# Optimization experiments

Hardware: AMD Instinct MI355X
Metric: run time of the kernel (lower is better)

The kernel has to match this reference:

```python
import jax, jax.numpy as jnp
import numpy as np

# Model constants (match init_kwargs + mamba_ssm defaults)
CIN, COUT, K, STRIDE = 64, 128, 4, 4
D = 128            # d_model = features_out
DI = 256           # d_inner = 2*D (expand=2)
NSTATE = 16        # d_state
DCONV = 4          # depthwise conv width
DT_RANK = 8        # ceil(D/16)
NB = 3             # blocks per direction
NTOT = 2 * NB      # forward + backward stacks


def setup_inputs() -> dict:
    key = jax.random.key(0)
    ks = jax.random.split(key, 10)
    s = 0.02
    x = jax.random.normal(ks[0], (2, CIN, 8192), jnp.float32)
    convd_w = jax.random.normal(ks[1], (COUT, CIN, K), jnp.float32) * s
    convd_b = jnp.zeros((COUT,), jnp.float32)
    ln_w = jnp.ones((NTOT, D), jnp.float32)
    ln_b = jnp.zeros((NTOT, D), jnp.float32)
    in_proj_w = jax.random.normal(ks[2], (NTOT, 2 * DI, D), jnp.float32) * s
    conv_w = jax.random.normal(ks[3], (NTOT, DI, DCONV), jnp.float32) * s
    conv_b = jnp.zeros((NTOT, DI), jnp.float32)
    xproj_w = jax.random.normal(ks[4], (NTOT, DT_RANK + 2 * NSTATE, DI), jnp.float32) * s
    dtproj_w = jax.random.normal(ks[5], (NTOT, DI, DT_RANK), jnp.float32) * s
    dtproj_b = jax.random.normal(ks[6], (NTOT, DI), jnp.float32) * s
    # S4D-real init: A = -[1..N]
    A_log = jnp.log(jnp.broadcast_to(jnp.arange(1, NSTATE + 1, dtype=jnp.float32), (NTOT, DI, NSTATE)))
    Dparam = jnp.ones((NTOT, DI), jnp.float32)
    outproj_w = jax.random.normal(ks[7], (NTOT, D, DI), jnp.float32) * s
    return dict(x=x, convd_w=convd_w, convd_b=convd_b, ln_w=ln_w, ln_b=ln_b,
                in_proj_w=in_proj_w, conv_w=conv_w, conv_b=conv_b, xproj_w=xproj_w,
                dtproj_w=dtproj_w, dtproj_b=dtproj_b, A_log=A_log, Dparam=Dparam,
                outproj_w=outproj_w)


def _silu(x):
    return x * jax.nn.sigmoid(x)


def _layernorm(x, w, b, eps=1e-5):
    m = x.mean(-1, keepdims=True)
    xc = x - m
    v = (xc * xc).mean(-1, keepdims=True)
    return xc * jax.lax.rsqrt(v + eps) * w + b


def _mamba_mixer(x, in_proj_w, conv_w, conv_b, xproj_w, dtproj_w, dtproj_b, A_log, Dp, outproj_w):
    # x: (B, L, D)
    B, L, _ = x.shape
    xz = jnp.einsum('bld,ed->ble', x, in_proj_w)          # (B, L, 2*DI)
    xm, z = jnp.split(xz, 2, axis=-1)
    # causal depthwise conv (pad left DCONV-1, truncate to L)
    xp = jnp.pad(xm, ((0, 0), (DCONV - 1, 0), (0, 0)))
    xc = conv_b
    acc = jnp.zeros_like(xm)
    for k in range(DCONV):
        acc = acc + xp[:, k:k + L, :] * conv_w[:, k]
    xc = _silu(acc + conv_b)                               # (B, L, DI)
    dbc = jnp.einsum('ble,ne->bln', xc, xproj_w)           # (B, L, DT_RANK + 2N)
    dt, Bc, Cc = jnp.split(dbc, [DT_RANK, DT_RANK + NSTATE], axis=-1)
    dt = jax.nn.softplus(jnp.einsum('blr,dr->bld', dt, dtproj_w) + dtproj_b)  # (B, L, DI)
    A = -jnp.exp(A_log)                                    # (DI, N)
    dA = jnp.exp(dt[..., None] * A)                        # (B, L, DI, N)
    dBx = dt[..., None] * Bc[:, :, None, :] * xc[..., None]

    def step(h, inp):
        dA_t, dBx_t, C_t = inp
        h = dA_t * h + dBx_t                               # (B, DI, N)
        y = jnp.einsum('bdn,bn->bd', h, C_t)
        return h, y

    h0 = jnp.zeros((B, DI, NSTATE), x.dtype)
    _, ys = jax.lax.scan(step, h0, (jnp.swapaxes(dA, 0, 1), jnp.swapaxes(dBx, 0, 1), jnp.swapaxes(Cc, 0, 1)))
    y = jnp.swapaxes(ys, 0, 1)                             # (B, L, DI)
    y = (y + Dp * xc) * _silu(z)
    return jnp.einsum('ble,de->bld', y, outproj_w)         # (B, L, D)


def _mamba_stack(x, off, ln_w, ln_b, in_proj_w, conv_w, conv_b, xproj_w, dtproj_w, dtproj_b, A_log, Dparam, outproj_w):
    # mamba_ssm Block semantics: residual = x (+ prev residual); x = mixer(norm(residual))
    res = None
    cur = x
    for i in range(NB):
        j = off + i
        res = cur if res is None else cur + res
        hn = _layernorm(res, ln_w[j], ln_b[j])
        cur = _mamba_mixer(hn, in_proj_w[j], conv_w[j], conv_b[j], xproj_w[j],
                           dtproj_w[j], dtproj_b[j], A_log[j], Dparam[j], outproj_w[j])
    return cur, res


def reference(x, convd_w, convd_b, ln_w, ln_b, in_proj_w, conv_w, conv_b, xproj_w,
              dtproj_w, dtproj_b, A_log, Dparam, outproj_w):
    # downsampling conv + SiLU
    y = jax.lax.conv_general_dilated(x, convd_w, (STRIDE,), 'VALID',
                                     dimension_numbers=('NCH', 'OIH', 'NCH'))
    y = _silu(y + convd_b[None, :, None])                  # (B, COUT, L')
    h = jnp.swapaxes(y, 1, 2)                              # (B, L', D)
    xf, rf = _mamba_stack(h, 0, ln_w, ln_b, in_proj_w, conv_w, conv_b, xproj_w,
                          dtproj_w, dtproj_b, A_log, Dparam, outproj_w)
    xb, rb = _mamba_stack(h[:, ::-1, :], NB, ln_w, ln_b, in_proj_w, conv_w, conv_b, xproj_w,
                          dtproj_w, dtproj_b, A_log, Dparam, outproj_w)
    out = (xf + rf) + (xb + rb)[:, ::-1, :]
    return jnp.swapaxes(out, 1, 2), rf, rb
```

## Files before the change

### kernel.cpp

```cpp
#include <hip/hip_runtime.h>
#include <hip/hip_bf16.h>
#include <math.h>

#define B    2
#define CIN  64
#define LIN  8192
#define L    2048
#define D    128
#define DI   256
#define NS   16
#define RK   8
#define NSTREAM 4
#define CH   32
#define NCH  (L/CH)
#define TOK  (NSTREAM*L)
#define SZ_D ((size_t)TOK*D)
#define SZ_DI ((size_t)TOK*DI)
#define SXM 280
#define SHN 152

typedef short  bfrag __attribute__((ext_vector_type(8)));
typedef float  facc  __attribute__((ext_vector_type(4)));
#define MFMA __builtin_amdgcn_mfma_f32_16x16x32_bf16

__device__ __forceinline__ float sigmoidf_(float x){ return 1.f/(1.f+__expf(-x)); }
__device__ __forceinline__ float siluf_(float x){ return x*sigmoidf_(x); }
__device__ __forceinline__ ushort f2bf(float f){
    unsigned u = __float_as_uint(f);
    u += 0x7fffu + ((u>>16)&1u);
    return (ushort)(u>>16);
}
__device__ __forceinline__ float bf2f(ushort u){ return __uint_as_float(((unsigned)u)<<16); }
__device__ __forceinline__ float softplusf_(float t){
    return (t > 20.f) ? t : __logf(1.f + __expf(t));
}

__global__ void k_cvtall(const float* __restrict__ cw, const float* __restrict__ ipw,
                         const float* __restrict__ opw, const float* __restrict__ xpw,
                         ushort* __restrict__ dst){
    int i = blockIdx.x*256 + threadIdx.x;
    ushort v;
    if (i < 32768)       v = f2bf(cw[i]);
    else if (i < 425984) v = f2bf(ipw[i-32768]);
    else if (i < 622592) v = f2bf(opw[i-425984]);
    else {
        int t = i - 622592;
        int k = t & 255, nr = (t>>8) & 63, j = t>>14;
        v = (nr < 40) ? f2bf(xpw[((size_t)j*40 + nr)*256 + k]) : (ushort)0;
    }
    dst[i] = v;
}

__global__ void k_down(const float* __restrict__ x, const ushort* __restrict__ wd,
                       const float* __restrict__ bias, float* __restrict__ h){
    __shared__ ushort sxd[64*SXM];
    int tid = threadIdx.x;
    int m0 = blockIdx.x*64;
    int b = m0 >> 11;
    int l0 = m0 & 2047;
    for (int idx = tid; idx < 64*64; idx += 256){
        int t = idx & 63, cc = idx >> 6;
        float4 v = *(const float4*)(x + ((size_t)(b*CIN + cc))*LIN + 4*(l0+t));
        ushort4 o; o.x=f2bf(v.x); o.y=f2bf(v.y); o.z=f2bf(v.z); o.w=f2bf(v.w);
        *(ushort4*)&sxd[t*SXM + cc*4] = o;
    }
    __syncthreads();
    int w = tid>>6, lane = tid&63, rw = w>>1, cw = w&1;
    int q = lane>>4, r = lane&15;
    int n0 = blockIdx.y*64 + cw*32;
    const ushort* b0p = wd + (size_t)(n0 + r)*256 + q*8;
    const ushort* b1p = b0p + (size_t)16*256;
    facc acc[2][2] = {};
    #pragma unroll
    for (int kb=0; kb<8; ++kb){
        bfrag a0 = *(bfrag*)&sxd[(rw*32 + r)*SXM + kb*32 + q*8];
        bfrag a1 = *(bfrag*)&sxd[(rw*32 + 16 + r)*SXM + kb*32 + q*8];
        bfrag b0 = *(const bfrag*)(b0p + kb*32);
        bfrag b1 = *(const bfrag*)(b1p + kb*32);
        acc[0][0] = MFMA(a0,b0,acc[0][0],0,0,0);
        acc[0][1] = MFMA(a0,b1,acc[0][1],0,0,0);
        acc[1][0] = MFMA(a1,b0,acc[1][0],0,0,0);
        acc[1][1] = MFMA(a1,b1,acc[1][1],0,0,0);
    }
    #pragma unroll
    for (int im=0; im<2; ++im)
    #pragma unroll
    for (int in=0; in<2; ++in){
        int col = n0 + in*16 + r;
        float bv = bias[col];
        #pragma unroll
        for (int r2=0; r2<4; ++r2){
            int row = m0 + rw*32 + im*16 + q*4 + r2;
            int bb = row >> 11, l = row & 2047;
            float v = siluf_(acc[im][in][r2] + bv);
            h[((size_t)(bb*L + l))*D + col] = v;
            h[((size_t)((2+bb)*L + (L-1-l)))*D + col] = v;
        }
    }
}

__global__ void __launch_bounds__(256,1)
k_head(const float* __restrict__ curIn, const float* __restrict__ resIn,
       float* __restrict__ resOut,
       const float* __restrict__ lnw, const float* __restrict__ lnb,
       const ushort* __restrict__ wbi, const ushort* __restrict__ wbx,
       const float* __restrict__ cw, const float* __restrict__ cb,
       const float* __restrict__ Wdt, const float* __restrict__ bdt,
       const float* __restrict__ A_log,
       float* __restrict__ z, float* __restrict__ xc,
       float* __restrict__ dtr, float* __restrict__ Bc, float* __restrict__ Cc,
       float* __restrict__ Aprod, float* __restrict__ Bend, int blk, int first){
    __shared__ ushort smHn[35*SHN];
    __shared__ ushort smXm[35*SXM];
    __shared__ ushort smXc[32*SXM];
    __shared__ float  smDbc[32*68];
    const int tid = threadIdx.x;
    const int bi = blockIdx.x;
    const int s = bi >> 6, c = bi & 63;
    const int j = (s>>1)*3 + blk;
    const int base_tok = s*L + c*CH;

    {
        int t = tid >> 3, g8 = tid & 7;
        size_t off = (size_t)(base_tok + t)*D + g8*16;
        float4 v[4];
        const float4* cp = (const float4*)(curIn + off);
        #pragma unroll
        for (int i=0;i<4;++i) v[i] = cp[i];
        if (!first){
            const float4* rp = (const float4*)(resIn + off);
            #pragma unroll
            for (int i=0;i<4;++i){ float4 rv=rp[i]; v[i].x+=rv.x; v[i].y+=rv.y; v[i].z+=rv.z; v[i].w+=rv.w; }
        }
        {
            float4* ro = (float4*)(resOut + off);
            #pragma unroll
            for (int i=0;i<4;++i) ro[i] = v[i];
        }
        float s1=0.f, s2=0.f;
        #pragma unroll
        for (int i=0;i<4;++i){
            s1 += v[i].x+v[i].y+v[i].z+v[i].w;
            s2 += v[i].x*v[i].x+v[i].y*v[i].y+v[i].z*v[i].z+v[i].w*v[i].w;
        }
        s1 += __shfl_xor(s1,1); s2 += __shfl_xor(s2,1);
        s1 += __shfl_xor(s1,2); s2 += __shfl_xor(s2,2);
        s1 += __shfl_xor(s1,4); s2 += __shfl_xor(s2,4);
        float mean = s1*(1.f/128.f);
        float var  = s2*(1.f/128.f) - mean*mean;
        float rstd = rsqrtf(var + 1e-5f);
        const float4* lwp = (const float4*)(lnw + j*D + g8*16);
        const float4* lbp = (const float4*)(lnb + j*D + g8*16);
        #pragma unroll
        for (int i=0;i<4;++i){
            float4 lw = lwp[i], lb = lbp[i];
            ushort4 o;
            o.x = f2bf((v[i].x-mean)*rstd*lw.x + lb.x);
            o.y = f2bf((v[i].y-mean)*rstd*lw.y + lb.y);
            o.z = f2bf((v[i].z-mean)*rstd*lw.z + lb.z);
            o.w = f2bf((v[i].w-mean)*rstd*lw.w + lb.w);
            *(ushort4*)&smHn[t*SHN + g8*16 + i*4] = o;
        }
    }
    if (c > 0 && tid < 24){
        int t = tid >> 3, g8 = tid & 7;
        size_t off = (size_t)(base_tok - 3 + t)*D + g8*16;
        float4 v[4];
        const float4* cp = (const float4*)(curIn + off);
        #pragma unroll
        for (int i=0;i<4;++i) v[i] = cp[i];
        if (!first){
            const float4* rp = (const float4*)(resIn + off);
            #pragma unroll
            for (int i=0;i<4;++i){ float4 rv=rp[i]; v[i].x+=rv.x; v[i].y+=rv.y; v[i].z+=rv.z; v[i].w+=rv.w; }
        }
        float s1=0.f, s2=0.f;
        #pragma unroll
        for (int i=0;i<4;++i){
            s1 += v[i].x+v[i].y+v[i].z+v[i].w;
            s2 += v[i].x*v[i].x+v[i].y*v[i].y+v[i].z*v[i].z+v[i].w*v[i].w;
        }
        s1 += __shfl_xor(s1,1); s2 += __shfl_xor(s2,1);
        s1 += __shfl_xor(s1,2); s2 += __shfl_xor(s2,2);
        s1 += __shfl_xor(s1,4); s2 += __shfl_xor(s2,4);
        float mean = s1*(1.f/128.f);
        float var  = s2*(1.f/128.f) - mean*mean;
        float rstd = rsqrtf(var + 1e-5f);
        const float4* lwp = (const float4*)(lnw + j*D + g8*16);
        const float4* lbp = (const float4*)(lnb + j*D + g8*16);
        #pragma unroll
        for (int i=0;i<4;++i){
            float4 lw = lwp[i], lb = lbp[i];
            ushort4 o;
            o.x = f2bf((v[i].x-mean)*rstd*lw.x + lb.x);
            o.y = f2bf((v[i].y-mean)*rstd*lw.y + lb.y);
            o.z = f2bf((v[i].z-mean)*rstd*lw.z + lb.z);
            o.w = f2bf((v[i].w-mean)*rstd*lw.w + lb.w);
            *(ushort4*)&smHn[(32+t)*SHN + g8*16 + i*4] = o;
        }
    }
    __syncthreads();

    {
        int w = tid>>6, lane = tid&63, q = lane>>4, r = lane&15;
        bfrag a[3][4];
        #pragma unroll
        for (int rt=0; rt<3; ++rt)
        #pragma unroll
        for (int kb=0; kb<4; ++kb)
            a[rt][kb] = *(bfrag*)&smHn[(rt*16 + r)*SHN + kb*32 + q*8];
        #pragma unroll
        for (int ct=0; ct<8; ++ct){
            int n0 = w*128 + ct*16;
            const ushort* bp = wbi + ((size_t)j*512 + n0 + r)*128 + q*8;
            facc a0 = {}, a1 = {}, a2 = {};
            #pragma unroll
            for (int kb=0; kb<4; ++kb){
                bfrag bv = *(const bfrag*)(bp + kb*32);
                a0 = MFMA(a[0][kb], bv, a0, 0,0,0);
                a1 = MFMA(a[1][kb], bv, a1, 0,0,0);
                a2 = MFMA(a[2][kb], bv, a2, 0,0,0);
            }
            int colL = n0 + r;
            if (colL < DI){
                #pragma unroll
                for (int r2=0;r2<4;++r2){
                    int rr = q*4 + r2;
                    smXm[rr*SXM + colL]      = f2bf(a0[r2]);
                    smXm[(16+rr)*SXM + colL] = f2bf(a1[r2]);
                    if (rr < 3) smXm[(32+rr)*SXM + colL] = f2bf(a2[r2]);
                }
            } else {
                int cz = colL - DI;
                #pragma unroll
                for (int r2=0;r2<4;++r2){
                    int rr = q*4 + r2;
                    z[(size_t)(base_tok + rr)*DI + cz]      = a0[r2];
                    z[(size_t)(base_tok + 16 + rr)*DI + cz] = a1[r2];
                }
            }
        }
    }
    __syncthreads();

    {
        const float* w4 = cw + ((size_t)j*DI + tid)*4;
        float cw0=w4[0], cw1=w4[1], cw2=w4[2], cw3=w4[3];
        float cbb = cb[j*DI + tid];
        float xm1=0.f, xm2=0.f, xm3=0.f;
        if (c > 0){
            xm3 = bf2f(smXm[32*SXM + tid]);
            xm2 = bf2f(smXm[33*SXM + tid]);
            xm1 = bf2f(smXm[34*SXM + tid]);
        }
        #pragma unroll 4
        for (int i=0;i<CH;++i){
            float x0 = bf2f(smXm[i*SXM + tid]);
            float v = siluf_(cbb + cw3*x0 + cw2*xm1 + cw1*xm2 + cw0*xm3);
            smXc[i*SXM + tid] = f2bf(v);
            xc[(size_t)(base_tok+i)*DI + tid] = v;
            xm3 = xm2; xm2 = xm1; xm1 = x0;
        }
    }
    __syncthreads();

    {
        int w = tid>>6, lane = tid&63, q = lane>>4, r = lane&15;
        facc a0 = {}, a1 = {};
        const ushort* bp = wbx + ((size_t)j*64 + w*16 + r)*256 + q*8;
        #pragma unroll
        for (int kb=0; kb<8; ++kb){
            bfrag av0 = *(bfrag*)&smXc[r*SXM + kb*32 + q*8];
            bfrag av1 = *(bfrag*)&smXc[(16+r)*SXM + kb*32 + q*8];
            bfrag bv  = *(const bfrag*)(bp + kb*32);
            a0 = MFMA(av0, bv, a0, 0,0,0);
            a1 = MFMA(av1, bv, a1, 0,0,0);
        }
        int col = w*16 + r;
        #pragma unroll
        for (int r2=0;r2<4;++r2){
            int rr = q*4 + r2;
            smDbc[rr*68 + col]      = a0[r2];
            smDbc[(16+rr)*68 + col] = a1[r2];
            int row0 = base_tok + rr, row1 = base_tok + 16 + rr;
            if      (col < 8){  dtr[(size_t)row0*RK + col] = a0[r2];      dtr[(size_t)row1*RK + col] = a1[r2]; }
            else if (col < 24){ Bc [(size_t)row0*NS + (col-8)] = a0[r2];  Bc [(size_t)row1*NS + (col-8)] = a1[r2]; }
            else if (col < 40){ Cc [(size_t)row0*NS + (col-24)] = a0[r2]; Cc [(size_t)row1*NS + (col-24)] = a1[r2]; }
        }
    }
    __syncthreads();

    {
        float A[NS], wv[RK];
        const float* ar = A_log + ((size_t)j*DI + tid)*NS;
        #pragma unroll
        for (int n=0;n<NS;++n) A[n] = -__expf(ar[n]);
        const float* wr = Wdt + ((size_t)j*DI + tid)*RK;
        #pragma unroll
        for (int r=0;r<RK;++r) wv[r] = wr[r];
        float bb2 = bdt[j*DI + tid];
        float ap[NS], hs[NS];
        #pragma unroll
        for (int n=0;n<NS;++n){ ap[n]=1.f; hs[n]=0.f; }
        #pragma unroll 4
        for (int l=0;l<CH;++l){
            float t = bb2;
            #pragma unroll
            for (int r=0;r<RK;++r) t += smDbc[l*68+r]*wv[r];
            float dtv = softplusf_(t);
            float xv  = bf2f(smXc[l*SXM + tid]);
            float dbx = dtv*xv;
            #pragma unroll
            for (int n=0;n<NS;++n){
                float dA = __expf(dtv*A[n]);
                ap[n] *= dA;
                hs[n] = dA*hs[n] + dbx*smDbc[l*68+8+n];
            }
        }
        size_t pb = (size_t)bi*4096 + tid;
        #pragma unroll
        for (int n=0;n<NS;++n){
            Aprod[pb + (size_t)n*256] = ap[n];
            Bend [pb + (size_t)n*256] = hs[n];
        }
    }
}

__global__ void k_scanmid(const float* __restrict__ Aprod, float* __restrict__ Bend){
    int tid = blockIdx.x*128 + threadIdx.x;
    int s = tid >> 12;
    int nd = tid & 4095;
    size_t base = (size_t)s*NCH*4096 + nd;
    float h = 0.f;
    for (int c0=0; c0<NCH; c0+=16){
        float a[16], b[16];
        #pragma unroll
        for (int i=0;i<16;++i){
            a[i] = Aprod[base + (size_t)(c0+i)*4096];
            b[i] = Bend [base + (size_t)(c0+i)*4096];
        }
        #pragma unroll
        for (int i=0;i<16;++i){
            Bend[base + (size_t)(c0+i)*4096] = h;
            h = a[i]*h + b[i];
        }
    }
}

__global__ void k_tail(const float* __restrict__ dtr, const float* __restrict__ xcv,
                       const float* __restrict__ Bc, const float* __restrict__ Cc,
                       const float* __restrict__ A_log,
                       const float* __restrict__ Wdt, const float* __restrict__ bdt,
                       const float* __restrict__ h0, const float* __restrict__ z,
                       const float* __restrict__ Dp, const ushort* __restrict__ wbo,
                       float* __restrict__ cur, int blk){
    int c = blockIdx.x, s = blockIdx.y; int j = (s>>1)*3 + blk;
    int d = threadIdx.x;
    __shared__ float sB[CH*NS], sC[CH*NS], sdtr[CH*RK];
    __shared__ ushort sg[CH*SXM];
    int base_tok = s*L + c*CH;
    sB[d] = Bc[(size_t)base_tok*NS + d];
    sB[256+d] = Bc[(size_t)base_tok*NS + 256 + d];
    sC[d] = Cc[(size_t)base_tok*NS + d];
    sC[256+d] = Cc[(size_t)base_tok*NS + 256 + d];
    sdtr[d] = dtr[(size_t)base_tok*RK + d];
    float A[NS], wv[RK];
    const float* ar = A_log + ((size_t)j*DI + d)*NS;
    #pragma unroll
    for (int n=0;n<NS;++n) A[n] = -__expf(ar[n]);
    const float* wr = Wdt + ((size_t)j*DI + d)*RK;
    #pragma unroll
    for (int r=0;r<RK;++r) wv[r] = wr[r];
    float bb = bdt[j*DI + d];
    float Dpd = Dp[j*DI + d];
    float hs[NS];
    size_t pb = (size_t)(s*NCH + c)*4096 + d;
    #pragma unroll
    for (int n=0;n<NS;++n) hs[n] = h0[pb + (size_t)n*256];
    __syncthreads();
    #pragma unroll 4
    for (int l=0;l<CH;++l){
        float t = bb;
        #pragma unroll
        for (int r=0;r<RK;++r) t += sdtr[l*RK+r]*wv[r];
        float dtv = softplusf_(t);
        float xv  = xcv[(size_t)(base_tok+l)*DI + d];
        float dbx = dtv*xv;
        float p = 0.f;
        #pragma unroll
        for (int n=0;n<NS;++n){
            float dA = __expf(dtv*A[n]);
            hs[n] = dA*hs[n] + dbx*sB[l*NS+n];
            p += hs[n]*sC[l*NS+n];
        }
        float zv = z[(size_t)(base_tok+l)*DI + d];
        sg[l*SXM + d] = f2bf((p + Dpd*xv)*siluf_(zv));
    }
    __syncthreads();
    int w = d>>6, lane = d&63, q = lane>>4, r = lane&15;
    facc acc[2][2] = {};
    const ushort* b0p = wbo + ((size_t)j*128 + w*32 + r)*256 + q*8;
    const ushort* b1p = b0p + 16*256;
    #pragma unroll
    for (int kb=0; kb<8; ++kb){
        bfrag av0 = *(bfrag*)&sg[r*SXM + kb*32 + q*8];
        bfrag av1 = *(bfrag*)&sg[(16+r)*SXM + kb*32 + q*8];
        bfrag bv0 = *(const bfrag*)(b0p + kb*32);
        bfrag bv1 = *(const bfrag*)(b1p + kb*32);
        acc[0][0] = MFMA(av0,bv0,acc[0][0],0,0,0);
        acc[0][1] = MFMA(av0,bv1,acc[0][1],0,0,0);
        acc[1][0] = MFMA(av1,bv0,acc[1][0],0,0,0);
        acc[1][1] = MFMA(av1,bv1,acc[1][1],0,0,0);
    }
    #pragma unroll
    for (int rt=0; rt<2; ++rt)
    #pragma unroll
    for (int ct=0; ct<2; ++ct){
        int col = w*32 + ct*16 + r;
        #pragma unroll
        for (int r2=0;r2<4;++r2){
            int row = base_tok + rt*16 + q*4 + r2;
            cur[(size_t)row*D + col] = acc[rt][ct][r2];
        }
    }
}

__global__ void k_final(const float* __restrict__ cur, const float* __restrict__ res,
                        float* __restrict__ out){
    int l = blockIdx.x, b = blockIdx.y, d = threadIdx.x;
    int tf = (b*L + l)*D + d;
    int tbk = ((2+b)*L + (L-1-l))*D + d;
    float f  = cur[tf] + res[tf];
    float bw = cur[tbk] + res[tbk];
    out[((size_t)(b*D + d))*L + l] = f + bw;
    out[(size_t)2*D*L + (size_t)(b*L + l)*D + d] = res[tf];
    out[(size_t)2*D*L + (size_t)((2+b)*L + l)*D + d] = res[((2+b)*L + l)*D + d];
}

extern "C" void kernel_launch(void* const* d_in, const int* in_sizes, int n_in,
                              void* d_out, int out_size, void* d_ws, size_t ws_size,
                              hipStream_t stream){
    const float* x         = (const float*)d_in[0];
    const float* convd_w   = (const float*)d_in[1];
    const float* convd_b   = (const float*)d_in[2];
    const float* ln_w      = (const float*)d_in[3];
    const float* ln_b      = (const float*)d_in[4];
    const float* in_proj_w = (const float*)d_in[5];
    const float* conv_w    = (const float*)d_in[6];
    const float* conv_b    = (const float*)d_in[7];
    const float* xproj_w   = (const float*)d_in[8];
    const float* dtproj_w  = (const float*)d_in[9];
    const float* dtproj_b  = (const float*)d_in[10];
    const float* A_log     = (const float*)d_in[11];
    const float* Dparam    = (const float*)d_in[12];
    const float* outproj_w = (const float*)d_in[13];

    float* ws = (float*)d_ws;
    float* h     = ws; ws += SZ_D;
    float* res0  = ws; ws += SZ_D;
    float* res1  = ws; ws += SZ_D;
    float* cur   = ws; ws += SZ_D;
    float* z     = ws; ws += SZ_DI;
    float* xc    = ws; ws += SZ_DI;
    float* Aprod = ws; ws += SZ_D;
    float* Bend  = ws; ws += SZ_D;
    float* dtr   = ws; ws += (size_t)TOK*RK;
    float* Bc    = ws; ws += (size_t)TOK*NS;
    float* Cc    = ws; ws += (size_t)TOK*NS;
    ushort* wall = (ushort*)ws;
    ushort* wbd  = wall;
    ushort* wbi  = wall + 32768;
    ushort* wbo  = wall + 425984;
    ushort* wbx  = wall + 622592;

    k_cvtall<<<2816, 256, 0, stream>>>(convd_w, in_proj_w, outproj_w, xproj_w, wall);
    k_down<<<dim3(64, 2), 256, 0, stream>>>(x, wbd, convd_b, h);

    float* resin[3]  = { nullptr, res0, res1 };
    float* resout[3] = { res0,    res1, res0 };
    for (int blk = 0; blk < 3; ++blk){
        const float* ci = (blk==0) ? h : cur;
        const float* ri = (blk==0) ? h : resin[blk];
        k_head<<<NSTREAM*NCH, 256, 0, stream>>>(ci, ri, resout[blk], ln_w, ln_b, wbi, wbx,
                                                conv_w, conv_b, dtproj_w, dtproj_b, A_log,
                                                z, xc, dtr, Bc, Cc, Aprod, Bend, blk, blk==0);
        k_scanmid<<<128, 128, 0, stream>>>(Aprod, Bend);
        k_tail<<<dim3(NCH, NSTREAM), 256, 0, stream>>>(dtr, xc, Bc, Cc, A_log,
                                                       dtproj_w, dtproj_b, Bend, z,
                                                       Dparam, wbo, cur, blk);
    }

    k_final<<<dim3(L, B), 128, 0, stream>>>(cur, res0, (float*)d_out);
}
```

Measured before the change: 256.2 us.

## Fuse all stages into one persistent kernel with grid-wide atomic barriers

Replaces the chain of separate launches (weight conversion, downsampling, per-block head/scan/tail, final) with one persistent 256-block kernel that separates stages with a software grid barrier built on an atomic counter. Some intermediates such as xc, dtr, Bc and Cc appear to stay in block-local shared memory rather than going through global buffers. This removes launch overhead and gaps between roughly a dozen small kernels. In exchange it relies on all 256 blocks being co-resident, pays for barrier spin time, and the barrier has a timeout break that could silently lose correctness.

```diff
diff --git a/kernel.cpp b/kernel.cpp
--- a/kernel.cpp
+++ b/kernel.cpp
@@ -1,5 +1,4 @@
 #include <hip/hip_runtime.h>
-#include <hip/hip_bf16.h>
 #include <math.h>
 
 #define B    2
@@ -35,460 +34,485 @@
     return (t > 20.f) ? t : __logf(1.f + __expf(t));
 }
 
-__global__ void k_cvtall(const float* __restrict__ cw, const float* __restrict__ ipw,
-                         const float* __restrict__ opw, const float* __restrict__ xpw,
-                         ushort* __restrict__ dst){
-    int i = blockIdx.x*256 + threadIdx.x;
-    ushort v;
-    if (i < 32768)       v = f2bf(cw[i]);
-    else if (i < 425984) v = f2bf(ipw[i-32768]);
-    else if (i < 622592) v = f2bf(opw[i-425984]);
-    else {
-        int t = i - 622592;
-        int k = t & 255, nr = (t>>8) & 63, j = t>>14;
-        v = (nr < 40) ? f2bf(xpw[((size_t)j*40 + nr)*256 + k]) : (ushort)0;
-    }
-    dst[i] = v;
-}
-
-__global__ void k_down(const float* __restrict__ x, const ushort* __restrict__ wd,
-                       const float* __restrict__ bias, float* __restrict__ h){
-    __shared__ ushort sxd[64*SXM];
-    int tid = threadIdx.x;
-    int m0 = blockIdx.x*64;
-    int b = m0 >> 11;
-    int l0 = m0 & 2047;
-    for (int idx = tid; idx < 64*64; idx += 256){
-        int t = idx & 63, cc = idx >> 6;
-        float4 v = *(const float4*)(x + ((size_t)(b*CIN + cc))*LIN + 4*(l0+t));
-        ushort4 o; o.x=f2bf(v.x); o.y=f2bf(v.y); o.z=f2bf(v.z); o.w=f2bf(v.w);
-        *(ushort4*)&sxd[t*SXM + cc*4] = o;
+__device__ __forceinline__ void gbar(unsigned* cnt, unsigned target){
+    __syncthreads();
+    if (threadIdx.x == 0){
+        __threadfence();
+        __hip_atomic_fetch_add(cnt, 1u, __ATOMIC_RELEASE, __HIP_MEMORY_SCOPE_AGENT);
+        unsigned guard = 0;
+        while (__hip_atomic_load(cnt, __ATOMIC_ACQUIRE, __HIP_MEMORY_SCOPE_AGENT) < target){
+            __builtin_amdgcn_s_sleep(8);
+            if (++guard > 4000000u) break;
+        }
+        __threadfence();
     }
     __syncthreads();
-    int w = tid>>6, lane = tid&63, rw = w>>1, cw = w&1;
-    int q = lane>>4, r = lane&15;
-    int n0 = blockIdx.y*64 + cw*32;
-    const ushort* b0p = wd + (size_t)(n0 + r)*256 + q*8;
-    const ushort* b1p = b0p + (size_t)16*256;
-    facc acc[2][2] = {};
-    #pragma unroll
-    for (int kb=0; kb<8; ++kb){
-        bfrag a0 = *(bfrag*)&sxd[(rw*32 + r)*SXM + kb*32 + q*8];
-        bfrag a1 = *(bfrag*)&sxd[(rw*32 + 16 + r)*SXM + kb*32 + q*8];
-        bfrag b0 = *(const bfrag*)(b0p + kb*32);
-        bfrag b1 = *(const bfrag*)(b1p + kb*32);
-        acc[0][0] = MFMA(a0,b0,acc[0][0],0,0,0);
-        acc[0][1] = MFMA(a0,b1,acc[0][1],0,0,0);
-        acc[1][0] = MFMA(a1,b0,acc[1][0],0,0,0);
-        acc[1][1] = MFMA(a1,b1,acc[1][1],0,0,0);
+}
+
+struct Params {
+    const float* __restrict__ x;
+    const float* __restrict__ convd_w;
+    const float* __restrict__ convd_b;
+    const float* __restrict__ ln_w;
+    const float* __restrict__ ln_b;
+    const float* __restrict__ in_proj_w;
+    const float* __restrict__ conv_w;
+    const float* __restrict__ conv_b;
+    const float* __restrict__ xproj_w;
+    const float* __restrict__ dtproj_w;
+    const float* __restrict__ dtproj_b;
+    const float* __restrict__ A_log;
+    const float* __restrict__ Dparam;
+    const float* __restrict__ outproj_w;
+    float* __restrict__ out;
+    float* __restrict__ h;
+    float* __restrict__ res0;
+    float* __restrict__ res1;
+    float* __restrict__ cur;
+    float* __restrict__ z;
+    float* __restrict__ Aprod;
+    float* __restrict__ Bend;
+    unsigned* __restrict__ bar;
+    ushort* __restrict__ wall;
+};
+
+__global__ void __launch_bounds__(256,1) k_fused(Params pr){
+    const int tid = threadIdx.x;
+    const int bid = blockIdx.x;
+    unsigned ep = 0;
+
+    __shared__ __align__(16) char smem[56864];
+    ushort* smHn  = (ushort*)smem;
+    ushort* smXm  = (ushort*)(smem + 10640);
+    ushort* smXc  = (ushort*)(smem + 30240);
+    float*  smDbc = (float*) (smem + 48160);
+    ushort* sg    = (ushort*)smem;
+    ushort* sxd   = (ushort*)smem;
+
+    ushort* wbd = pr.wall;
+    ushort* wbi = pr.wall + 32768;
+    ushort* wbo = pr.wall + 425984;
+    ushort* wbx = pr.wall + 622592;
+
+    {
+        int g = bid*256 + tid;
+        for (int i = g; i < 720896; i += 65536){
+            ushort v;
+            if (i < 32768)       v = f2bf(pr.convd_w[i]);
+            else if (i < 425984) v = f2bf(pr.in_proj_w[i-32768]);
+            else if (i < 622592) v = f2bf(pr.outproj_w[i-425984]);
+            else {
+                int t = i - 622592;
+                int k = t & 255, nr = (t>>8) & 63, jj = t>>14;
+                v = (nr < 40) ? f2bf(pr.xproj_w[((size_t)jj*40 + nr)*256 + k]) : (ushort)0;
+            }
+            pr.wall[i] = v;
+        }
     }
-    #pragma unroll
-    for (int im=0; im<2; ++im)
-    #pragma unroll
-    for (int in=0; in<2; ++in){
-        int col = n0 + in*16 + r;
-        float bv = bias[col];
-        #pragma unroll
-        for (int r2=0; r2<4; ++r2){
-            int row = m0 + rw*32 + im*16 + q*4 + r2;
-            int bb = row >> 11, l = row & 2047;
-            float v = siluf_(acc[im][in][r2] + bv);
-            h[((size_t)(bb*L + l))*D + col] = v;
-            h[((size_t)((2+bb)*L + (L-1-l)))*D + col] = v;
-        }
-    }
-}
-
-__global__ void __launch_bounds__(256,1)
-k_head(const float* __restrict__ curIn, const float* __restrict__ resIn,
-       float* __restrict__ resOut,
-       const float* __restrict__ lnw, const float* __restrict__ lnb,
-       const ushort* __restrict__ wbi, const ushort* __restrict__ wbx,
-       const float* __restrict__ cw, const float* __restrict__ cb,
-       const float* __restrict__ Wdt, const float* __restrict__ bdt,
-       const float* __restrict__ A_log,
-       float* __restrict__ z, float* __restrict__ xc,
-       float* __restrict__ dtr, float* __restrict__ Bc, float* __restrict__ Cc,
-       float* __restrict__ Aprod, float* __restrict__ Bend, int blk, int first){
-    __shared__ ushort smHn[35*SHN];
-    __shared__ ushort smXm[35*SXM];
-    __shared__ ushort smXc[32*SXM];
-    __shared__ float  smDbc[32*68];
-    const int tid = threadIdx.x;
-    const int bi = blockIdx.x;
-    const int s = bi >> 6, c = bi & 63;
-    const int j = (s>>1)*3 + blk;
-    const int base_tok = s*L + c*CH;
-
-    {
-        int t = tid >> 3, g8 = tid & 7;
-        size_t off = (size_t)(base_tok + t)*D + g8*16;
-        float4 v[4];
-        const float4* cp = (const float4*)(curIn + off);
-        #pragma unroll
-        for (int i=0;i<4;++i) v[i] = cp[i];
-        if (!first){
-            const float4* rp = (const float4*)(resIn + off);
-            #pragma unroll
-            for (int i=0;i<4;++i){ float4 rv=rp[i]; v[i].x+=rv.x; v[i].y+=rv.y; v[i].z+=rv.z; v[i].w+=rv.w; }
-        }
-        {
-            float4* ro = (float4*)(resOut + off);
-            #pragma unroll
-            for (int i=0;i<4;++i) ro[i] = v[i];
-        }
-        float s1=0.f, s2=0.f;
-        #pragma unroll
-        for (int i=0;i<4;++i){
-            s1 += v[i].x+v[i].y+v[i].z+v[i].w;
-            s2 += v[i].x*v[i].x+v[i].y*v[i].y+v[i].z*v[i].z+v[i].w*v[i].w;
-        }
-        s1 += __shfl_xor(s1,1); s2 += __shfl_xor(s2,1);
-        s1 += __shfl_xor(s1,2); s2 += __shfl_xor(s2,2);
-        s1 += __shfl_xor(s1,4); s2 += __shfl_xor(s2,4);
-        float mean = s1*(1.f/128.f);
-        float var  = s2*(1.f/128.f) - mean*mean;
-        float rstd = rsqrtf(var + 1e-5f);
-        const float4* lwp = (const float4*)(lnw + j*D + g8*16);
-        const float4* lbp = (const float4*)(lnb + j*D + g8*16);
-        #pragma unroll
-        for (int i=0;i<4;++i){
-            float4 lw = lwp[i], lb = lbp[i];
-            ushort4 o;
-            o.x = f2bf((v[i].x-mean)*rstd*lw.x + lb.x);
-            o.y = f2bf((v[i].y-mean)*rstd*lw.y + lb.y);
-            o.z = f2bf((v[i].z-mean)*rstd*lw.z + lb.z);
-            o.w = f2bf((v[i].w-mean)*rstd*lw.w + lb.w);
-            *(ushort4*)&smHn[t*SHN + g8*16 + i*4] = o;
-        }
-    }
-    if (c > 0 && tid < 24){
-        int t = tid >> 3, g8 = tid & 7;
-        size_t off = (size_t)(base_tok - 3 + t)*D + g8*16;
-        float4 v[4];
-        const float4* cp = (const float4*)(curIn + off);
-        #pragma unroll
-        for (int i=0;i<4;++i) v[i] = cp[i];
-        if (!first){
-            const float4* rp = (const float4*)(resIn + off);
-            #pragma unroll
-            for (int i=0;i<4;++i){ float4 rv=rp[i]; v[i].x+=rv.x; v[i].y+=rv.y; v[i].z+=rv.z; v[i].w+=rv.w; }
-        }
-        float s1=0.f, s2=0.f;
-        #pragma unroll
-        for (int i=0;i<4;++i){
-            s1 += v[i].x+v[i].y+v[i].z+v[i].w;
-            s2 += v[i].x*v[i].x+v[i].y*v[i].y+v[i].z*v[i].z+v[i].w*v[i].w;
-        }
-        s1 += __shfl_xor(s1,1); s2 += __shfl_xor(s2,1);
-        s1 += __shfl_xor(s1,2); s2 += __shfl_xor(s2,2);
-        s1 += __shfl_xor(s1,4); s2 += __shfl_xor(s2,4);
-        float mean = s1*(1.f/128.f);
-        float var  = s2*(1.f/128.f) - mean*mean;
-        float rstd = rsqrtf(var + 1e-5f);
-        const float4* lwp = (const float4*)(lnw + j*D + g8*16);
-        const float4* lbp = (const float4*)(lnb + j*D + g8*16);
-        #pragma unroll
-        for (int i=0;i<4;++i){
-            float4 lw = lwp[i], lb = lbp[i];
-            ushort4 o;
-            o.x = f2bf((v[i].x-mean)*rstd*lw.x + lb.x);
-            o.y = f2bf((v[i].y-mean)*rstd*lw.y + lb.y);
-            o.z = f2bf((v[i].z-mean)*rstd*lw.z + lb.z);
-            o.w = f2bf((v[i].w-mean)*rstd*lw.w + lb.w);
-            *(ushort4*)&smHn[(32+t)*SHN + g8*16 + i*4] = o;
-        }
-    }
-    __syncthreads();
-
-    {
-        int w = tid>>6, lane = tid&63, q = lane>>4, r = lane&15;
-        bfrag a[3][4];
-        #pragma unroll
-        for (int rt=0; rt<3; ++rt)
-        #pragma unroll
-        for (int kb=0; kb<4; ++kb)
-            a[rt][kb] = *(bfrag*)&smHn[(rt*16 + r)*SHN + kb*32 + q*8];
-        #pragma unroll
-        for (int ct=0; ct<8; ++ct){
-            int n0 = w*128 + ct*16;
-            const ushort* bp = wbi + ((size_t)j*512 + n0 + r)*128 + q*8;
-            facc a0 = {}, a1 = {}, a2 = {};
-            #pragma unroll
-            for (int kb=0; kb<4; ++kb){
-                bfrag bv = *(const bfrag*)(bp + kb*32);
-                a0 = MFMA(a[0][kb], bv, a0, 0,0,0);
-                a1 = MFMA(a[1][kb], bv, a1, 0,0,0);
-                a2 = MFMA(a[2][kb], bv, a2, 0,0,0);
-            }
-            int colL = n0 + r;
-            if (colL < DI){
-                #pragma unroll
-                for (int r2=0;r2<4;++r2){
-                    int rr = q*4 + r2;
-                    smXm[rr*SXM + colL]      = f2bf(a0[r2]);
-                    smXm[(16+rr)*SXM + colL] = f2bf(a1[r2]);
-                    if (rr < 3) smXm[(32+rr)*SXM + colL] = f2bf(a2[r2]);
-                }
-            } else {
-                int cz = colL - DI;
-                #pragma unroll
-                for (int r2=0;r2<4;++r2){
-                    int rr = q*4 + r2;
-                    z[(size_t)(base_tok + rr)*DI + cz]      = a0[r2];
-                    z[(size_t)(base_tok + 16 + rr)*DI + cz] = a1[r2];
-                }
-            }
-        }
-    }
-    __syncthreads();
-
-    {
-        const float* w4 = cw + ((size_t)j*DI + tid)*4;
-        float cw0=w4[0], cw1=w4[1], cw2=w4[2], cw3=w4[3];
-        float cbb = cb[j*DI + tid];
-        float xm1=0.f, xm2=0.f, xm3=0.f;
-        if (c > 0){
-            xm3 = bf2f(smXm[32*SXM + tid]);
-            xm2 = bf2f(smXm[33*SXM + tid]);
-            xm1 = bf2f(smXm[34*SXM + tid]);
-        }
-        #pragma unroll 4
-        for (int i=0;i<CH;++i){
-            float x0 = bf2f(smXm[i*SXM + tid]);
-            float v = siluf_(cbb + cw3*x0 + cw2*xm1 + cw1*xm2 + cw0*xm3);
-            smXc[i*SXM + tid] = f2bf(v);
-            xc[(size_t)(base_tok+i)*DI + tid] = v;
-            xm3 = xm2; xm2 = xm1; xm1 = x0;
-        }
-    }
-    __syncthreads();
-
-    {
-        int w = tid>>6, lane = tid&63, q = lane>>4, r = lane&15;
-        facc a0 = {}, a1 = {};
-        const ushort* bp = wbx + ((size_t)j*64 + w*16 + r)*256 + q*8;
+    gbar(pr.bar, (++ep)*256u);
+
+    if (bid < 128){
+        int mb = bid & 63, nb = bid >> 6;
+        int m0 = mb*64;
+        int bb_ = m0 >> 11;
+        int l0 = m0 & 2047;
+        for (int idx = tid; idx < 64*64; idx += 256){
+            int t = idx & 63, cc = idx >> 6;
+            float4 v = *(const float4*)(pr.x + ((size_t)(bb_*CIN + cc))*LIN + 4*(l0+t));
+            ushort4 o; o.x=f2bf(v.x); o.y=f2bf(v.y); o.z=f2bf(v.z); o.w=f2bf(v.w);
+            *(ushort4*)&sxd[t*SXM + cc*4] = o;
+        }
+        __syncthreads();
+        int w = tid>>6, lane = tid&63, rw = w>>1, cw_ = w&1;
+        int q = lane>>4, r = lane&15;
+        int n0 = nb*64 + cw_*32;
+        const ushort* b0p = wbd + (size_t)(n0 + r)*256 + q*8;
+        const ushort* b1p = b0p + (size_t)16*256;
+        facc acc[2][2] = {};
         #pragma unroll
         for (int kb=0; kb<8; ++kb){
-            bfrag av0 = *(bfrag*)&smXc[r*SXM + kb*32 + q*8];
-            bfrag av1 = *(bfrag*)&smXc[(16+r)*SXM + kb*32 + q*8];
-            bfrag bv  = *(const bfrag*)(bp + kb*32);
-            a0 = MFMA(av0, bv, a0, 0,0,0);
-            a1 = MFMA(av1, bv, a1, 0,0,0);
-        }
-        int col = w*16 + r;
+            bfrag a0 = *(bfrag*)&sxd[(rw*32 + r)*SXM + kb*32 + q*8];
+            bfrag a1 = *(bfrag*)&sxd[(rw*32 + 16 + r)*SXM + kb*32 + q*8];
+            bfrag b0 = *(const bfrag*)(b0p + kb*32);
+            bfrag b1 = *(const bfrag*)(b1p + kb*32);
+            acc[0][0] = MFMA(a0,b0,acc[0][0],0,0,0);
+            acc[0][1] = MFMA(a0,b1,acc[0][1],0,0,0);
+            acc[1][0] = MFMA(a1,b0,acc[1][0],0,0,0);
+            acc[1][1] = MFMA(a1,b1,acc[1][1],0,0,0);
+        }
         #pragma unroll
-        for (int r2=0;r2<4;++r2){
-            int rr = q*4 + r2;
-            smDbc[rr*68 + col]      = a0[r2];
-            smDbc[(16+rr)*68 + col] = a1[r2];
-            int row0 = base_tok + rr, row1 = base_tok + 16 + rr;
-            if      (col < 8){  dtr[(size_t)row0*RK + col] = a0[r2];      dtr[(size_t)row1*RK + col] = a1[r2]; }
-            else if (col < 24){ Bc [(size_t)row0*NS + (col-8)] = a0[r2];  Bc [(size_t)row1*NS + (col-8)] = a1[r2]; }
-            else if (col < 40){ Cc [(size_t)row0*NS + (col-24)] = a0[r2]; Cc [(size_t)row1*NS + (col-24)] = a1[r2]; }
+        for (int im=0; im<2; ++im)
+        #pragma unroll
+        for (int in=0; in<2; ++in){
+            int col = n0 + in*16 + r;
+            float bv = pr.convd_b[col];
+            #pragma unroll
+            for (int r2=0; r2<4; ++r2){
+                int row = m0 + rw*32 + im*16 + q*4 + r2;
+                int bb2 = row >> 11, l = row & 2047;
+                float v = siluf_(acc[im][in][r2] + bv);
+                pr.h[((size_t)(bb2*L + l))*D + col] = v;
+                pr.h[((size_t)((2+bb2)*L + (L-1-l)))*D + col] = v;
+            }
         }
     }
-    __syncthreads();
+    gbar(pr.bar, (++ep)*256u);
+
+    const int s = bid >> 6, c = bid & 63;
+    const int base_tok = s*L + c*CH;
+
+    for (int blk = 0; blk < 3; ++blk){
+        const int j = (s>>1)*3 + blk;
+        const int first = (blk==0);
+        const float* curIn = first ? pr.h : pr.cur;
+        const float* resIn = (blk==0) ? pr.h : ((blk==1) ? pr.res0 : pr.res1);
+        float* resOut = (blk==1) ? pr.res1 : pr.res0;
+
+        {
+            int t = tid >> 3, g8 = tid & 7;
+            size_t off = (size_t)(base_tok + t)*D + g8*16;
+            float4 v[4];
+            const float4* cp = (const float4*)(curIn + off);
+            #pragma unroll
+            for (int i=0;i<4;++i) v[i] = cp[i];
+            if (!first){
+                const float4* rp = (const float4*)(resIn + off);
+                #pragma unroll
+                for (int i=0;i<4;++i){ float4 rv=rp[i]; v[i].x+=rv.x; v[i].y+=rv.y; v[i].z+=rv.z; v[i].w+=rv.w; }
+            }
+            {
+                float4* ro = (float4*)(resOut + off);
+                #pragma unroll
+                for (int i=0;i<4;++i) ro[i] = v[i];
+            }
+            float s1=0.f, s2=0.f;
+            #pragma unroll
+            for (int i=0;i<4;++i){
+                s1 += v[i].x+v[i].y+v[i].z+v[i].w;
+                s2 += v[i].x*v[i].x+v[i].y*v[i].y+v[i].z*v[i].z+v[i].w*v[i].w;
+            }
+            s1 += __shfl_xor(s1,1); s2 += __shfl_xor(s2,1);
+            s1 += __shfl_xor(s1,2); s2 += __shfl_xor(s2,2);
+            s1 += __shfl_xor(s1,4); s2 += __shfl_xor(s2,4);
+            float mean = s1*(1.f/128.f);
+            float var  = s2*(1.f/128.f) - mean*mean;
+            float rstd = rsqrtf(var + 1e-5f);
+            const float4* lwp = (const float4*)(pr.ln_w + j*D + g8*16);
+            const float4* lbp = (const float4*)(pr.ln_b + j*D + g8*16);
+            #pragma unroll
+            for (int i=0;i<4;++i){
+                float4 lw = lwp[i], lb = lbp[i];
+                ushort4 o;
+                o.x = f2bf((v[i].x-mean)*rstd*lw.x + lb.x);
+                o.y = f2bf((v[i].y-mean)*rstd*lw.y + lb.y);
+                o.z = f2bf((v[i].z-mean)*rstd*lw.z + lb.z);
+                o.w = f2bf((v[i].w-mean)*rstd*lw.w + lb.w);
+                *(ushort4*)&smHn[t*SHN + g8*16 + i*4] = o;
+            }
+        }
+        if (c > 0 && tid < 24){
+            int t = tid >> 3, g8 = tid & 7;
+            size_t off = (size_t)(base_tok - 3 + t)*D + g8*16;
+            float4 v[4];
+            const float4* cp = (const float4*)(curIn + off);
+            #pragma unroll
+            for (int i=0;i<4;++i) v[i] = cp[i];
+            if (!first){
+                const float4* rp = (const float4*)(resIn + off);
+                #pragma unroll
+                for (int i=0;i<4;++i){ float4 rv=rp[i]; v[i].x+=rv.x; v[i].y+=rv.y; v[i].z+=rv.z; v[i].w+=rv.w; }
+            }
+            float s1=0.f, s2=0.f;
+            #pragma unroll
+            for (int i=0;i<4;++i){
+                s1 += v[i].x+v[i].y+v[i].z+v[i].w;
+                s2 += v[i].x*v[i].x+v[i].y*v[i].y+v[i].z*v[i].z+v[i].w*v[i].w;
+            }
+            s1 += __shfl_xor(s1,1); s2 += __shfl_xor(s2,1);
+            s1 += __shfl_xor(s1,2); s2 += __shfl_xor(s2,2);
+            s1 += __shfl_xor(s1,4); s2 += __shfl_xor(s2,4);
+            float mean = s1*(1.f/128.f);
+            float var  = s2*(1.f/128.f) - mean*mean;
+            float rstd = rsqrtf(var + 1e-5f);
+            const float4* lwp = (const float4*)(pr.ln_w + j*D + g8*16);
+            const float4* lbp = (const float4*)(pr.ln_b + j*D + g8*16);
+            #pragma unroll
+            for (int i=0;i<4;++i){
+                float4 lw = lwp[i], lb = lbp[i];
+                ushort4 o;
+                o.x = f2bf((v[i].x-mean)*rstd*lw.x + lb.x);
+                o.y = f2bf((v[i].y-mean)*rstd*lw.y + lb.y);
+                o.z = f2bf((v[i].z-mean)*rstd*lw.z + lb.z);
+                o.w = f2bf((v[i].w-mean)*rstd*lw.w + lb.w);
+                *(ushort4*)&smHn[(32+t)*SHN + g8*16 + i*4] = o;
+            }
+        }
+        __syncthreads();
+
+        {
+            int w = tid>>6, lane = tid&63, q = lane>>4, r = lane&15;
+            bfrag a[3][4];
+            #pragma unroll
+            for (int rt=0; rt<3; ++rt)
+            #pragma unroll
+            for (int kb=0; kb<4; ++kb)
+                a[rt][kb] = *(bfrag*)&smHn[(rt*16 + r)*SHN + kb*32 + q*8];
+            #pragma unroll
+            for (int ct=0; ct<8; ++ct){
+                int n0 = w*128 + ct*16;
+                const ushort* bp = wbi + ((size_t)j*512 + n0 + r)*128 + q*8;
+                facc a0 = {}, a1 = {}, a2 = {};
+                #pragma unroll
+                for (int kb=0; kb<4; ++kb){
+                    bfrag bv = *(const bfrag*)(bp + kb*32);
+                    a0 = MFMA(a[0][kb], bv, a0, 0,0,0);
+                    a1 = MFMA(a[1][kb], bv, a1, 0,0,0);
+                    a2 = MFMA(a[2][kb], bv, a2, 0,0,0);
+                }
+                int colL = n0 + r;
+                if (colL < DI){
+                    #pragma unroll
+                    for (int r2=0;r2<4;++r2){
+                        int rr = q*4 + r2;
+                        smXm[rr*SXM + colL]      = f2bf(a0[r2]);
+                        smXm[(16+rr)*SXM + colL] = f2bf(a1[r2]);
+                        if (rr < 3) smXm[(32+rr)*SXM + colL] = f2bf(a2[r2]);
+                    }
+                } else {
+                    int cz = colL - DI;
+                    #pragma unroll
+                    for (int r2=0;r2<4;++r2){
+                        int rr = q*4 + r2;
+                        pr.z[(size_t)(base_tok + rr)*DI + cz]      = a0[r2];
+                        pr.z[(size_t)(base_tok + 16 + rr)*DI + cz] = a1[r2];
+                    }
+                }
+            }
+        }
+        __syncthreads();
+
+        {
+            const float* w4 = pr.conv_w + ((size_t)j*DI + tid)*4;
+            float cw0=w4[0], cw1=w4[1], cw2=w4[2], cw3=w4[3];
+            float cbb = pr.conv_b[j*DI + tid];
+            float xm1=0.f, xm2=0.f, xm3=0.f;
+            if (c > 0){
+                xm3 = bf2f(smXm[32*SXM + tid]);
+                xm2 = bf2f(smXm[33*SXM + tid]);
+                xm1 = bf2f(smXm[34*SXM + tid]);
+            }
+            #pragma unroll 4
+            for (int i=0;i<CH;++i){
+                float x0 = bf2f(smXm[i*SXM + tid]);
+                float v = siluf_(cbb + cw3*x0 + cw2*xm1 + cw1*xm2 + cw0*xm3);
+                smXc[i*SXM + tid] = f2bf(v);
+                xm3 = xm2; xm2 = xm1; xm1 = x0;
+            }
+        }
+        __syncthreads();
+
+        {
+            int w = tid>>6, lane = tid&63, q = lane>>4, r = lane&15;
+            facc a0 = {}, a1 = {};
+            const ushort* bp = wbx + ((size_t)j*64 + w*16 + r)*256 + q*8;
+            #pragma unroll
+            for (int kb=0; kb<8; ++kb){
+                bfrag av0 = *(bfrag*)&smXc[r*SXM + kb*32 + q*8];
+                bfrag av1 = *(bfrag*)&smXc[(16+r)*SXM + kb*32 + q*8];
+                bfrag bv  = *(const bfrag*)(bp + kb*32);
+                a0 = MFMA(av0, bv, a0, 0,0,0);
+                a1 = MFMA(av1, bv, a1, 0,0,0);
+            }
+            int col = w*16 + r;
+            #pragma unroll
+            for (int r2=0;r2<4;++r2){
+                int rr = q*4 + r2;
+                smDbc[rr*68 + col]      = a0[r2];
+                smDbc[(16+rr)*68 + col] = a1[r2];
+            }
+        }
+        __syncthreads();
+
+        {
+            float A[NS], wv[RK];
+            const float* ar = pr.A_log + ((size_t)j*DI + tid)*NS;
+            #pragma unroll
+            for (int n=0;n<NS;++n) A[n] = -__expf(ar[n]);
+            const float* wr = pr.dtproj_w + ((size_t)j*DI + tid)*RK;
+            #pragma unroll
+            for (int r=0;r<RK;++r) wv[r] = wr[r];
+            float bb2 = pr.dtproj_b[j*DI + tid];
+            float ap[NS], hs[NS];
+            #pragma unroll
+            for (int n=0;n<NS;++n){ ap[n]=1.f; hs[n]=0.f; }
+            #pragma unroll 4
+            for (int l=0;l<CH;++l){
+                float t = bb2;
+                #pragma unroll
+                for (int r=0;r<RK;++r) t += smDbc[l*68+r]*wv[r];
+                float dtv = softplusf_(t);
+                float xv  = bf2f(smXc[l*SXM + tid]);
+                float dbx = dtv*xv;
+                #pragma unroll
+                for (int n=0;n<NS;++n){
+                    float dA = __expf(dtv*A[n]);
+                    ap[n] *= dA;
+                    hs[n] = dA*hs[n] + dbx*smDbc[l*68+8+n];
+                }
+            }
+            size_t pb = (size_t)bid*4096 + tid;
+            #pragma unroll
+            for (int n=0;n<NS;++n){
+                pr.Aprod[pb + (size_t)n*256] = ap[n];
+                pr.Bend [pb + (size_t)n*256] = hs[n];
+            }
+        }
+        gbar(pr.bar, (++ep)*256u);
+
+        {
+            int g = bid*256 + tid;
+            int q = g & 3;
+            int lane2 = g >> 2;
+            int ss = lane2 >> 12, nd = lane2 & 4095;
+            size_t base = (size_t)ss*NCH*4096 + nd;
+            float a[16], b[16];
+            #pragma unroll
+            for (int i=0;i<16;++i){
+                a[i] = pr.Aprod[base + (size_t)(q*16+i)*4096];
+                b[i] = pr.Bend [base + (size_t)(q*16+i)*4096];
+            }
+            float Aag = 1.f, Bag = 0.f;
+            #pragma unroll
+            for (int i=0;i<16;++i){ Bag = a[i]*Bag + b[i]; Aag *= a[i]; }
+            int lid = tid & 63, gb = lid & ~3;
+            float hcar = 0.f;
+            #pragma unroll
+            for (int pq = 0; pq < 3; ++pq){
+                float aA = __shfl(Aag, gb + pq, 64);
+                float aB = __shfl(Bag, gb + pq, 64);
+                if (pq < q) hcar = aA*hcar + aB;
+            }
+            #pragma unroll
+            for (int i=0;i<16;++i){
+                pr.Bend[base + (size_t)(q*16+i)*4096] = hcar;
+                hcar = a[i]*hcar + b[i];
+            }
+        }
+        gbar(pr.bar, (++ep)*256u);
+
+        {
+            const int d = tid;
+            float A[NS], wv[RK];
+            const float* ar = pr.A_log + ((size_t)j*DI + d)*NS;
+            #pragma unroll
+            for (int n=0;n<NS;++n) A[n] = -__expf(ar[n]);
+            const float* wr = pr.dtproj_w + ((size_t)j*DI + d)*RK;
+            #pragma unroll
+            for (int r=0;r<RK;++r) wv[r] = wr[r];
+            float bb = pr.dtproj_b[j*DI + d];
+            float Dpd = pr.Dparam[j*DI + d];
+            float hs[NS];
+            size_t pb = (size_t)bid*4096 + d;
+            #pragma unroll
+            for (int n=0;n<NS;++n) hs[n] = pr.Bend[pb + (size_t)n*256];
+            #pragma unroll 4
+            for (int l=0;l<CH;++l){
+                float t = bb;
+                #pragma unroll
+                for (int r=0;r<RK;++r) t += smDbc[l*68+r]*wv[r];
+                float dtv = softplusf_(t);
+                float xv  = bf2f(smXc[l*SXM + d]);
+                float dbx = dtv*xv;
+                float pacc = 0.f;
+                #pragma unroll
+                for (int n=0;n<NS;++n){
+                    float dA = __expf(dtv*A[n]);
+                    hs[n] = dA*hs[n] + dbx*smDbc[l*68+8+n];
+                    pacc += hs[n]*smDbc[l*68+24+n];
+                }
+                float zv = pr.z[(size_t)(base_tok+l)*DI + d];
+                sg[l*SXM + d] = f2bf((pacc + Dpd*xv)*siluf_(zv));
+            }
+            __syncthreads();
+            int w = d>>6, lane = d&63, q = lane>>4, r = lane&15;
+            facc acc[2][2] = {};
+            const ushort* b0p = wbo + ((size_t)j*128 + w*32 + r)*256 + q*8;
+            const ushort* b1p = b0p + 16*256;
+            #pragma unroll
+            for (int kb=0; kb<8; ++kb){
+                bfrag av0 = *(bfrag*)&sg[r*SXM + kb*32 + q*8];
+                bfrag av1 = *(bfrag*)&sg[(16+r)*SXM + kb*32 + q*8];
+                bfrag bv0 = *(const bfrag*)(b0p + kb*32);
+                bfrag bv1 = *(const bfrag*)(b1p + kb*32);
+                acc[0][0] = MFMA(av0,bv0,acc[0][0],0,0,0);
+                acc[0][1] = MFMA(av0,bv1,acc[0][1],0,0,0);
+                acc[1][0] = MFMA(av1,bv0,acc[1][0],0,0,0);
+                acc[1][1] = MFMA(av1,bv1,acc[1][1],0,0,0);
+            }
+            #pragma unroll
+            for (int rt=0; rt<2; ++rt)
+            #pragma unroll
+            for (int ct=0; ct<2; ++ct){
+                int col = w*32 + ct*16 + r;
+                #pragma unroll
+                for (int r2=0;r2<4;++r2){
+                    int row = base_tok + rt*16 + q*4 + r2;
+                    pr.cur[(size_t)row*D + col] = acc[rt][ct][r2];
+                }
+            }
+        }
+        gbar(pr.bar, (++ep)*256u);
+    }
 
     {
-        float A[NS], wv[RK];
-        const float* ar = A_log + ((size_t)j*DI + tid)*NS;
-        #pragma unroll
-        for (int n=0;n<NS;++n) A[n] = -__expf(ar[n]);
-        const float* wr = Wdt + ((size_t)j*DI + tid)*RK;
-        #pragma unroll
-        for (int r=0;r<RK;++r) wv[r] = wr[r];
-        float bb2 = bdt[j*DI + tid];
-        float ap[NS], hs[NS];
-        #pragma unroll
-        for (int n=0;n<NS;++n){ ap[n]=1.f; hs[n]=0.f; }
-        #pragma unroll 4
-        for (int l=0;l<CH;++l){
-            float t = bb2;
-            #pragma unroll
-            for (int r=0;r<RK;++r) t += smDbc[l*68+r]*wv[r];
-            float dtv = softplusf_(t);
-            float xv  = bf2f(smXc[l*SXM + tid]);
-            float dbx = dtv*xv;
-            #pragma unroll
-            for (int n=0;n<NS;++n){
-                float dA = __expf(dtv*A[n]);
-                ap[n] *= dA;
-                hs[n] = dA*hs[n] + dbx*smDbc[l*68+8+n];
-            }
-        }
-        size_t pb = (size_t)bi*4096 + tid;
-        #pragma unroll
-        for (int n=0;n<NS;++n){
-            Aprod[pb + (size_t)n*256] = ap[n];
-            Bend [pb + (size_t)n*256] = hs[n];
+        int g = bid*256 + tid;
+        for (int idx = g; idx < 524288; idx += 65536){
+            int d = idx & 127, l = (idx >> 7) & 2047, bb_ = idx >> 18;
+            int tf  = (bb_*L + l)*D + d;
+            int tbk = ((2+bb_)*L + (L-1-l))*D + d;
+            float f  = pr.cur[tf] + pr.res0[tf];
+            float bw = pr.cur[tbk] + pr.res0[tbk];
+            pr.out[((size_t)(bb_*D + d))*L + l] = f + bw;
+            pr.out[(size_t)2*D*L + (size_t)(bb_*L + l)*D + d] = pr.res0[tf];
+            pr.out[(size_t)2*D*L + (size_t)((2+bb_)*L + l)*D + d] = pr.res0[((2+bb_)*L + l)*D + d];
         }
     }
-}
-
-__global__ void k_scanmid(const float* __restrict__ Aprod, float* __restrict__ Bend){
-    int tid = blockIdx.x*128 + threadIdx.x;
-    int s = tid >> 12;
-    int nd = tid & 4095;
-    size_t base = (size_t)s*NCH*4096 + nd;
-    float h = 0.f;
-    for (int c0=0; c0<NCH; c0+=16){
-        float a[16], b[16];
-        #pragma unroll
-        for (int i=0;i<16;++i){
-            a[i] = Aprod[base + (size_t)(c0+i)*4096];
-            b[i] = Bend [base + (size_t)(c0+i)*4096];
-        }
-        #pragma unroll
-        for (int i=0;i<16;++i){
-            Bend[base + (size_t)(c0+i)*4096] = h;
-            h = a[i]*h + b[i];
-        }
-    }
-}
-
-__global__ void k_tail(const float* __restrict__ dtr, const float* __restrict__ xcv,
-                       const float* __restrict__ Bc, const float* __restrict__ Cc,
-                       const float* __restrict__ A_log,
-                       const float* __restrict__ Wdt, const float* __restrict__ bdt,
-                       const float* __restrict__ h0, const float* __restrict__ z,
-                       const float* __restrict__ Dp, const ushort* __restrict__ wbo,
-                       float* __restrict__ cur, int blk){
-    int c = blockIdx.x, s = blockIdx.y; int j = (s>>1)*3 + blk;
-    int d = threadIdx.x;
-    __shared__ float sB[CH*NS], sC[CH*NS], sdtr[CH*RK];
-    __shared__ ushort sg[CH*SXM];
-    int base_tok = s*L + c*CH;
-    sB[d] = Bc[(size_t)base_tok*NS + d];
-    sB[256+d] = Bc[(size_t)base_tok*NS + 256 + d];
-    sC[d] = Cc[(size_t)base_tok*NS + d];
-    sC[256+d] = Cc[(size_t)base_tok*NS + 256 + d];
-    sdtr[d] = dtr[(size_t)base_tok*RK + d];
-    float A[NS], wv[RK];
-    const float* ar = A_log + ((size_t)j*DI + d)*NS;
-    #pragma unroll
-    for (int n=0;n<NS;++n) A[n] = -__expf(ar[n]);
-    const float* wr = Wdt + ((size_t)j*DI + d)*RK;
-    #pragma unroll
-    for (int r=0;r<RK;++r) wv[r] = wr[r];
-    float bb = bdt[j*DI + d];
-    float Dpd = Dp[j*DI + d];
-    float hs[NS];
-    size_t pb = (size_t)(s*NCH + c)*4096 + d;
-    #pragma unroll
-    for (int n=0;n<NS;++n) hs[n] = h0[pb + (size_t)n*256];
-    __syncthreads();
-    #pragma unroll 4
-    for (int l=0;l<CH;++l){
-        float t = bb;
-        #pragma unroll
-        for (int r=0;r<RK;++r) t += sdtr[l*RK+r]*wv[r];
-        float dtv = softplusf_(t);
-        float xv  = xcv[(size_t)(base_tok+l)*DI + d];
-        float dbx = dtv*xv;
-        float p = 0.f;
-        #pragma unroll
-        for (int n=0;n<NS;++n){
-            float dA = __expf(dtv*A[n]);
-            hs[n] = dA*hs[n] + dbx*sB[l*NS+n];
-            p += hs[n]*sC[l*NS+n];
-        }
-        float zv = z[(size_t)(base_tok+l)*DI + d];
-        sg[l*SXM + d] = f2bf((p + Dpd*xv)*siluf_(zv));
-    }
-    __syncthreads();
-    int w = d>>6, lane = d&63, q = lane>>4, r = lane&15;
-    facc acc[2][2] = {};
-    const ushort* b0p = wbo + ((size_t)j*128 + w*32 + r)*256 + q*8;
-    const ushort* b1p = b0p + 16*256;
-    #pragma unroll
-    for (int kb=0; kb<8; ++kb){
-        bfrag av0 = *(bfrag*)&sg[r*SXM + kb*32 + q*8];
-        bfrag av1 = *(bfrag*)&sg[(16+r)*SXM + kb*32 + q*8];
-        bfrag bv0 = *(const bfrag*)(b0p + kb*32);
-        bfrag bv1 = *(const bfrag*)(b1p + kb*32);
-        acc[0][0] = MFMA(av0,bv0,acc[0][0],0,0,0);
-        acc[0][1] = MFMA(av0,bv1,acc[0][1],0,0,0);
-        acc[1][0] = MFMA(av1,bv0,acc[1][0],0,0,0);
-        acc[1][1] = MFMA(av1,bv1,acc[1][1],0,0,0);
-    }
-    #pragma unroll
-    for (int rt=0; rt<2; ++rt)
-    #pragma unroll
-    for (int ct=0; ct<2; ++ct){
-        int col = w*32 + ct*16 + r;
-        #pragma unroll
-        for (int r2=0;r2<4;++r2){
-            int row = base_tok + rt*16 + q*4 + r2;
-            cur[(size_t)row*D + col] = acc[rt][ct][r2];
-        }
-    }
-}
-
-__global__ void k_final(const float* __restrict__ cur, const float* __restrict__ res,
-                        float* __restrict__ out){
-    int l = blockIdx.x, b = blockIdx.y, d = threadIdx.x;
-    int tf = (b*L + l)*D + d;
-    int tbk = ((2+b)*L + (L-1-l))*D + d;
-    float f  = cur[tf] + res[tf];
-    float bw = cur[tbk] + res[tbk];
-    out[((size_t)(b*D + d))*L + l] = f + bw;
-    out[(size_t)2*D*L + (size_t)(b*L + l)*D + d] = res[tf];
-    out[(size_t)2*D*L + (size_t)((2+b)*L + l)*D + d] = res[((2+b)*L + l)*D + d];
 }
 
 extern "C" void kernel_launch(void* const* d_in, const int* in_sizes, int n_in,
                               void* d_out, int out_size, void* d_ws, size_t ws_size,
                               hipStream_t stream){
-    const float* x         = (const float*)d_in[0];
-    const float* convd_w   = (const float*)d_in[1];
-    const float* convd_b   = (const float*)d_in[2];
-    const float* ln_w      = (const float*)d_in[3];
-    const float* ln_b      = (const float*)d_in[4];
-    const float* in_proj_w = (const float*)d_in[5];
-    const float* conv_w    = (const float*)d_in[6];
-    const float* conv_b    = (const float*)d_in[7];
-    const float* xproj_w   = (const float*)d_in[8];
-    const float* dtproj_w  = (const float*)d_in[9];
-    const float* dtproj_b  = (const float*)d_in[10];
-    const float* A_log     = (const float*)d_in[11];
-    const float* Dparam    = (const float*)d_in[12];
-    const float* outproj_w = (const float*)d_in[13];
+    (void)in_sizes; (void)n_in; (void)out_size; (void)ws_size;
+    Params pr;
+    pr.x         = (const float*)d_in[0];
+    pr.convd_w   = (const float*)d_in[1];
+    pr.convd_b   = (const float*)d_in[2];
+    pr.ln_w      = (const float*)d_in[3];
+    pr.ln_b      = (const float*)d_in[4];
+    pr.in_proj_w = (const float*)d_in[5];
+    pr.conv_w    = (const float*)d_in[6];
+    pr.conv_b    = (const float*)d_in[7];
+    pr.xproj_w   = (const float*)d_in[8];
+    pr.dtproj_w  = (const float*)d_in[9];
+    pr.dtproj_b  = (const float*)d_in[10];
+    pr.A_log     = (const float*)d_in[11];
+    pr.Dparam    = (const float*)d_in[12];
+    pr.outproj_w = (const float*)d_in[13];
+    pr.out       = (float*)d_out;
 
     float* ws = (float*)d_ws;
-    float* h     = ws; ws += SZ_D;
-    float* res0  = ws; ws += SZ_D;
-    float* res1  = ws; ws += SZ_D;
-    float* cur   = ws; ws += SZ_D;
-    float* z     = ws; ws += SZ_DI;
-    float* xc    = ws; ws += SZ_DI;
-    float* Aprod = ws; ws += SZ_D;
-    float* Bend  = ws; ws += SZ_D;
-    float* dtr   = ws; ws += (size_t)TOK*RK;
-    float* Bc    = ws; ws += (size_t)TOK*NS;
-    float* Cc    = ws; ws += (size_t)TOK*NS;
-    ushort* wall = (ushort*)ws;
-    ushort* wbd  = wall;
-    ushort* wbi  = wall + 32768;
-    ushort* wbo  = wall + 425984;
-    ushort* wbx  = wall + 622592;
-
-    k_cvtall<<<2816, 256, 0, stream>>>(convd_w, in_proj_w, outproj_w, xproj_w, wall);
-    k_down<<<dim3(64, 2), 256, 0, stream>>>(x, wbd, convd_b, h);
-
-    float* resin[3]  = { nullptr, res0, res1 };
-    float* resout[3] = { res0,    res1, res0 };
-    for (int blk = 0; blk < 3; ++blk){
-        const float* ci = (blk==0) ? h : cur;
-        const float* ri = (blk==0) ? h : resin[blk];
-        k_head<<<NSTREAM*NCH, 256, 0, stream>>>(ci, ri, resout[blk], ln_w, ln_b, wbi, wbx,
-                                                conv_w, conv_b, dtproj_w, dtproj_b, A_log,
-                                                z, xc, dtr, Bc, Cc, Aprod, Bend, blk, blk==0);
-        k_scanmid<<<128, 128, 0, stream>>>(Aprod, Bend);
-        k_tail<<<dim3(NCH, NSTREAM), 256, 0, stream>>>(dtr, xc, Bc, Cc, A_log,
-                                                       dtproj_w, dtproj_b, Bend, z,
-                                                       Dparam, wbo, cur, blk);
-    }
-
-    k_final<<<dim3(L, B), 128, 0, stream>>>(cur, res0, (float*)d_out);
+    pr.h     = ws; ws += SZ_D;
+    pr.res0  = ws; ws += SZ_D;
+    pr.res1  = ws; ws += SZ_D;
+    pr.cur   = ws; ws += SZ_D;
+    pr.z     = ws; ws += SZ_DI;
+    ws += SZ_DI;
+    pr.Aprod = ws; ws += SZ_D;
+    pr.Bend  = ws; ws += SZ_D;
+    pr.bar   = (unsigned*)ws;
+    ws += (size_t)TOK*RK + 2*(size_t)TOK*NS;
+    pr.wall  = (ushort*)ws;
+
+    hipMemsetAsync((void*)pr.bar, 0, 16, stream);
+    hipLaunchKernelGGL(k_fused, dim3(256), dim3(256), 0, stream, pr);
 }
```

Result: slower. 642.7 us (+150.9%).
